# Kernel tuning notes

Measured on AMD Instinct MI355X. Metric: run time of the kernel, lower is better.

Reference implementation:

```python
import jax, jax.numpy as jnp
import numpy as np

B, N, C = 8, 2_000_000, 16


def _per_batch_loss(x, t, num_classes):
    """x: [N] float values, t: [N] int labels.
    For each label group: loss = mean(group) - mode(group) (scipy mode,
    ties -> smallest value), scattered back to every position of that label.
    """
    n = x.shape[0]
    # Sort primarily by label, secondarily by value (lexsort: last key primary).
    order = jnp.lexsort((x, t))
    xs = x[order]
    ts = t[order]
    # Run-length encode equal (label, value) pairs to count value multiplicity.
    new_run = jnp.concatenate(
        [jnp.ones((1,), bool), (ts[1:] != ts[:-1]) | (xs[1:] != xs[:-1])])
    run_id = jnp.cumsum(new_run) - 1                      # [N]
    run_cnt = jax.ops.segment_sum(jnp.ones(n, xs.dtype), run_id,
                                  num_segments=n)[run_id]  # count per element
    # Mode per label = smallest value attaining the max multiplicity.
    grp_max = jax.ops.segment_max(run_cnt, ts, num_segments=num_classes)
    mode = jax.ops.segment_min(
        jnp.where(run_cnt == grp_max[ts], xs, jnp.inf), ts,
        num_segments=num_classes)                         # [C]
    ssum = jax.ops.segment_sum(xs, ts, num_segments=num_classes)
    scnt = jax.ops.segment_sum(jnp.ones(n, xs.dtype), ts,
                               num_segments=num_classes)
    mean = ssum / jnp.maximum(scnt, 1.0)
    per_label = jnp.where(scnt > 0, mean - mode, 0.0)     # [C]
    return per_label[t]                                    # scatter back, [N]


def setup_inputs() -> dict:
    key = jax.random.key(0)
    k1, k2 = jax.random.split(key)
    inputs = jax.random.normal(k1, (B, N), dtype=jnp.float32)
    targets = jax.random.randint(k2, (B, N), 0, C, dtype=jnp.int32)
    return {"inputs": inputs, "targets": targets, "num_classes": C}


def reference(inputs, targets, num_classes):
    per_pos = jax.vmap(lambda x, t: _per_batch_loss(x, t, num_classes))(
        inputs, targets)                                   # [B, N]
    return jnp.mean(per_pos)
```

## Files before the change

### kernel.cpp

```cpp
#include <hip/hip_runtime.h>
#include <stdint.h>

#define NUM_C 16
#define NUM_B 8
#define NBKT (NUM_C * 64)
#define NGRP 256
#define CHUNK_S 4096
#define TAB 4096
#define MAX_NB 8

__device__ __forceinline__ unsigned hash_u32(unsigned h) {
    h ^= h >> 16; h *= 0x85ebca6bu;
    h ^= h >> 13; h *= 0xc2b2ae35u;
    h ^= h >> 16;
    return h;
}
__device__ __forceinline__ unsigned canon_key(float v) {
    unsigned k = __float_as_uint(v);
    return (k == 0x80000000u) ? 0u : k;
}
__device__ __forceinline__ unsigned bucket_of(unsigned key, int c) {
    return ((unsigned)c << 6) | (hash_u32(key) >> 26);
}

__global__ void __launch_bounds__(512)
sort_kernel(const float* __restrict__ x, const int* __restrict__ t,
            long long N, int bbase, int nchunk,
            unsigned* __restrict__ keysout, unsigned short* __restrict__ offs)
{
    __shared__ unsigned hist[NBKT];
    __shared__ unsigned lout[CHUNK_S];
    __shared__ unsigned wsum[8];
    const int lb = blockIdx.x / nchunk;
    const int ch = blockIdx.x % nchunk;
    const int b  = bbase + lb;
    const long long base = (long long)ch * CHUNK_S;
    const int count = (int)((N - base < CHUNK_S) ? (N - base) : CHUNK_S);
    const float* xb = x + (size_t)b * N + base;
    const int*   tb = t + (size_t)b * N + base;
    const int tid = threadIdx.x;

    for (int i = tid; i < NBKT; i += 512) hist[i] = 0u;
    __syncthreads();

    unsigned keys[8], pk[8];
    const int n4 = count >> 2;
    #pragma unroll
    for (int r = 0; r < 2; ++r) {
        const int idx4 = tid + r * 512;
        if (idx4 < n4) {
            float4 v  = ((const float4*)xb)[idx4];
            int4   cc = ((const int4*)tb)[idx4];
            unsigned k0 = canon_key(v.x), b0 = bucket_of(k0, cc.x);
            unsigned k1 = canon_key(v.y), b1 = bucket_of(k1, cc.y);
            unsigned k2 = canon_key(v.z), b2 = bucket_of(k2, cc.z);
            unsigned k3 = canon_key(v.w), b3 = bucket_of(k3, cc.w);
            unsigned p0 = atomicAdd(&hist[b0], 1u);
            unsigned p1 = atomicAdd(&hist[b1], 1u);
            unsigned p2 = atomicAdd(&hist[b2], 1u);
            unsigned p3 = atomicAdd(&hist[b3], 1u);
            keys[r*4+0] = k0; pk[r*4+0] = (b0 << 13) | p0;
            keys[r*4+1] = k1; pk[r*4+1] = (b1 << 13) | p1;
            keys[r*4+2] = k2; pk[r*4+2] = (b2 << 13) | p2;
            keys[r*4+3] = k3; pk[r*4+3] = (b3 << 13) | p3;
        }
    }
    unsigned kex = 0u, pkx = 0u; int hex = 0;
    {
        const int remi = (n4 << 2) + tid;
        if (remi < count) {
            unsigned k = canon_key(xb[remi]);
            unsigned bk = bucket_of(k, tb[remi]);
            unsigned p = atomicAdd(&hist[bk], 1u);
            kex = k; pkx = (bk << 13) | p; hex = 1;
        }
    }
    __syncthreads();

    {
        unsigned b0v = hist[2 * tid], b1v = hist[2 * tid + 1];
        unsigned s = b0v + b1v, inc = s;
        const int lane = tid & 63;
        #pragma unroll
        for (int d = 1; d < 64; d <<= 1) {
            unsigned tt = __shfl_up(inc, d);
            if (lane >= d) inc += tt;
        }
        if (lane == 63) wsum[tid >> 6] = inc;
        __syncthreads();
        unsigned wbase = 0;
        for (int i = 0; i < (tid >> 6); ++i) wbase += wsum[i];
        unsigned excl = wbase + inc - s;
        hist[2 * tid]     = excl + b0v;
        hist[2 * tid + 1] = excl + s;
        __syncthreads();
    }

    #pragma unroll
    for (int r = 0; r < 2; ++r) {
        const int idx4 = tid + r * 512;
        if (idx4 < n4) {
            #pragma unroll
            for (int c2 = 0; c2 < 4; ++c2) {
                unsigned bk = pk[r*4+c2] >> 13, p = pk[r*4+c2] & 8191u;
                lout[(bk ? hist[bk - 1] : 0u) + p] = keys[r*4+c2];
            }
        }
    }
    if (hex) {
        unsigned bk = pkx >> 13, p = pkx & 8191u;
        lout[(bk ? hist[bk - 1] : 0u) + p] = kex;
    }
    __syncthreads();

    unsigned* kb = keysout + (size_t)lb * N + base;
    if (count == CHUNK_S) {
        #pragma unroll
        for (int r = 0; r < 2; ++r)
            ((uint4*)kb)[tid + r * 512] = ((const uint4*)lout)[tid + r * 512];
    } else {
        for (int i = tid; i < count; i += 512) kb[i] = lout[i];
    }
    unsigned short* orow = offs + ((size_t)lb * nchunk + ch) * 1025;
    orow[tid]       = (unsigned short)(tid ? hist[tid - 1] : 0u);
    orow[tid + 512] = (unsigned short)hist[tid + 511];
    if (tid == 0) orow[1024] = (unsigned short)hist[1023];
}

__global__ void __launch_bounds__(256)
transpose_kernel(const unsigned short* __restrict__ offs,
                 unsigned short* __restrict__ offsT, int nchunk, int nchpad)
{
    __shared__ unsigned short tile[32][33];
    const int tiles_r = 33;
    const int tiles_c = (nchunk + 31) >> 5;
    const int lb  = blockIdx.x / (tiles_r * tiles_c);
    const int rem = blockIdx.x % (tiles_r * tiles_c);
    const int r0 = (rem / tiles_c) * 32;
    const int c0 = (rem % tiles_c) * 32;
    const unsigned short* src = offs + (size_t)lb * nchunk * 1025;
    unsigned short* dst = offsT + (size_t)lb * 1025 * nchpad;
    const int tx = threadIdx.x & 31, ty = threadIdx.x >> 5;

    #pragma unroll
    for (int dy = 0; dy < 32; dy += 8) {
        int ch = c0 + ty + dy, row = r0 + tx;
        tile[ty + dy][tx] = (ch < nchunk && row < 1025)
            ? src[(size_t)ch * 1025 + row] : (unsigned short)0;
    }
    __syncthreads();
    #pragma unroll
    for (int dy = 0; dy < 32; dy += 8) {
        int row = r0 + ty + dy, ch = c0 + tx;
        if (row < 1025 && ch < nchpad)
            dst[(size_t)row * nchpad + ch] = tile[tx][ty + dy];
    }
}

__global__ void __launch_bounds__(512)
mode_kernel(const unsigned* __restrict__ keysout,
            const unsigned short* __restrict__ offsT,
            long long N, int nchunk, int nchpad, int bbase,
            unsigned long long* __restrict__ best,
            double* __restrict__ psum,
            unsigned* __restrict__ pcnt)
{
    __shared__ unsigned keyt[TAB];
    __shared__ unsigned cnt16[TAB / 2];
    __shared__ unsigned short rowbuf[5][512];
    __shared__ unsigned long long redb[8];
    __shared__ double reds[8];
    __shared__ unsigned redc[8];

    const unsigned nwg = gridDim.x;
    const unsigned logical = (blockIdx.x & 7u) * (nwg >> 3) + (blockIdx.x >> 3);
    const unsigned lb = logical >> 8;
    const unsigned G  = logical & 255u;
    const unsigned g0 = G << 2;
    const unsigned c  = G >> 4;
    const unsigned b  = (unsigned)bbase + lb;
    const int tid = threadIdx.x;
    const int lane = tid & 63, wid = tid >> 6;

    const uint4 z4 = make_uint4(0u, 0u, 0u, 0u);
    for (int i = tid; i < TAB / 4; i += 512) ((uint4*)keyt)[i] = z4;
    for (int i = tid; i < TAB / 8; i += 512) ((uint4*)cnt16)[i] = z4;

    const unsigned short* obT = offsT + (size_t)lb * 1025 * nchpad;
    for (int i = tid; i < 5 * 512; i += 512) {
        int r = i >> 9, q = i & 511;
        rowbuf[r][q] = (q < nchunk)
            ? obT[(size_t)(g0 + r) * nchpad + q] : (unsigned short)0;
    }
    __syncthreads();

    const unsigned* kb = keysout + (size_t)lb * N;
    double ls = 0.0;
    unsigned mo = 0xFFFFFFFFu;
    unsigned lc = 0u;
    unsigned bc = 0u, bo = 0xFFFFFFFFu;

    const int nit = (nchunk + 127) >> 7;
    for (int sb = 0; sb < 4; ++sb) {
        for (int it = 0; it < nit; ++it) {
            const int q = it * 128 + wid * 16 + (lane >> 2);
            if (q < nchunk) {
                const unsigned s = rowbuf[sb][q];
                const unsigned e = rowbuf[sb + 1][q];
                const unsigned* src = kb + (size_t)q * CHUNK_S;
                for (unsigned jj = s + (unsigned)(lane & 3); jj < e; jj += 4u) {
                    unsigned key = src[jj];
                    ls += (double)__uint_as_float(key);
                    ++lc;
                    unsigned o = (key & 0x80000000u) ? ~key
                                                     : (key | 0x80000000u);
                    if (o < mo) mo = o;
                    unsigned hh = hash_u32(o) & (TAB - 1);
                    unsigned old = atomicCAS(&keyt[hh], 0u, o);
                    unsigned cnt = 1u;
                    while (old != 0u) {
                        if (old == o) {
                            unsigned sh = (hh & 1u) << 4;
                            unsigned ret =
                                atomicAdd(&cnt16[hh >> 1], 1u << sh);
                            cnt = ((ret >> sh) & 0xFFFFu) + 2u;
                            break;
                        }
                        hh = (hh + 1u) & (TAB - 1u);
                        old = atomicCAS(&keyt[hh], 0u, o);
                    }
                    if (cnt >= 2u && (cnt > bc || (cnt == bc && o < bo))) {
                        bc = cnt; bo = o;
                    }
                }
            }
        }
        if (sb < 3) {
            __syncthreads();
            for (int i = tid; i < TAB / 4; i += 512) ((uint4*)keyt)[i] = z4;
            for (int i = tid; i < TAB / 8; i += 512) ((uint4*)cnt16)[i] = z4;
            __syncthreads();
        }
    }

    unsigned long long lbst = bc ? (((unsigned long long)bc << 32)
                                    | (unsigned long long)(~bo)) : 0ull;
    {
        unsigned long long s1 = (1ull << 32) | (unsigned long long)(~mo);
        if (s1 > lbst) lbst = s1;
    }
    #pragma unroll
    for (int sh = 32; sh > 0; sh >>= 1) {
        unsigned long long obv = __shfl_down(lbst, sh);
        if (obv > lbst) lbst = obv;
        ls += __shfl_down(ls, sh);
        lc += __shfl_down(lc, sh);
    }
    if (lane == 0) { redb[wid] = lbst; reds[wid] = ls; redc[wid] = lc; }
    __syncthreads();
    if (tid == 0) {
        unsigned long long bb = 0ull; double ss = 0.0; unsigned cc = 0u;
        #pragma unroll
        for (int i = 0; i < 8; ++i) {
            if (redb[i] > bb) bb = redb[i];
            ss += reds[i];
            cc += redc[i];
        }
        psum[b * NGRP + G] = ss;
        pcnt[b * NGRP + G] = cc;
        if (bb) atomicMax(&best[b * NUM_C + c], bb);
    }
}

__global__ void __launch_bounds__(128)
finalize_kernel(const double* __restrict__ psum,
                const unsigned* __restrict__ pcnt,
                const unsigned long long* __restrict__ best,
                float* __restrict__ out, double inv_total)
{
    __shared__ double acc[NUM_B * NUM_C];
    const int i = threadIdx.x;
    const int b = i >> 4, c = i & 15;

    double s = 0.0;
    unsigned long long cnt = 0ull;
    const double*   ps = psum + (size_t)b * NGRP + ((size_t)c << 4);
    const unsigned* pc = pcnt + (size_t)b * NGRP + ((size_t)c << 4);
    for (int r = 0; r < 16; ++r) { s += ps[r]; cnt += pc[r]; }

    double term = 0.0;
    if (cnt > 0ull) {
        unsigned long long p = best[i];
        unsigned ord = 0xFFFFFFFFu - (unsigned)(p & 0xFFFFFFFFull);
        unsigned ub  = (ord & 0x80000000u) ? (ord ^ 0x80000000u) : ~ord;
        float mode = __uint_as_float(ub);
        term = s - (double)cnt * (double)mode;
    }
    acc[i] = term;
    __syncthreads();
    for (int st = 64; st > 0; st >>= 1) {
        if (i < st) acc[i] += acc[i + st];
        __syncthreads();
    }
    if (i == 0) out[0] = (float)(acc[0] * inv_total);
}

extern "C" void kernel_launch(void* const* d_in, const int* in_sizes, int n_in,
                              void* d_out, int out_size, void* d_ws, size_t ws_size,
                              hipStream_t stream)
{
    const float* x = (const float*)d_in[0];
    const int*   t = (const int*)d_in[1];

    const long long total = in_sizes[0];
    const long long N = total / NUM_B;
    const int nchunk = (int)((N + CHUNK_S - 1) / CHUNK_S);
    const int nchpad = (nchunk + 63) & ~63;

    char* ws = (char*)d_ws;
    size_t off = 0;
    unsigned long long* best = (unsigned long long*)(ws + off);
    off += (size_t)NUM_B * NUM_C * 8;
    double* psum = (double*)(ws + off);
    off += (size_t)NUM_B * NGRP * 8;
    unsigned* pcnt = (unsigned*)(ws + off);
    off += (size_t)NUM_B * NGRP * 4;
    off = (off + 255) & ~(size_t)255;

    const size_t keys_per_b  = (size_t)N * 4;
    const size_t offs_per_b  = (size_t)nchunk * 1025 * 2;
    const size_t offsT_per_b = (size_t)1025 * nchpad * 2;
    const size_t per_b = keys_per_b + offs_per_b + offsT_per_b + 512;
    size_t remaining = ws_size - off;
    int nb = (int)(remaining / per_b);
    if (nb < 1) nb = 1;
    if (nb > MAX_NB) nb = MAX_NB;
    {
        int rounds = (NUM_B + nb - 1) / nb;
        nb = (NUM_B + rounds - 1) / rounds;
    }

    unsigned* keysout = (unsigned*)(ws + off);
    off += (size_t)nb * keys_per_b;
    off = (off + 255) & ~(size_t)255;
    unsigned short* offsA = (unsigned short*)(ws + off);
    off += (size_t)nb * offs_per_b;
    off = (off + 255) & ~(size_t)255;
    unsigned short* offsT = (unsigned short*)(ws + off);
    off += (size_t)nb * offsT_per_b;

    const int tiles = 33 * ((nchunk + 31) >> 5);
    hipMemsetAsync(best, 0, (size_t)NUM_B * NUM_C * 8, stream);
    for (int r = 0; r < NUM_B; r += nb) {
        const int nbr = (NUM_B - r < nb) ? (NUM_B - r) : nb;
        sort_kernel<<<nbr * nchunk, 512, 0, stream>>>(
            x, t, N, r, nchunk, keysout, offsA);
        transpose_kernel<<<nbr * tiles, 256, 0, stream>>>(
            offsA, offsT, nchunk, nchpad);
        mode_kernel<<<nbr * NGRP, 512, 0, stream>>>(
            keysout, offsT, N, nchunk, nchpad, r, best, psum, pcnt);
    }
    finalize_kernel<<<1, 128, 0, stream>>>(
        psum, pcnt, best, (float*)d_out,
        1.0 / ((double)NUM_B * (double)N));
}
```

Before: 276.6 us.

## Use larger hash table with two sub-bucket passes and one thread per chunk

The mode kernel's shared hash table doubles to 8192 slots. Each work-group now handles its four sub-buckets in two passes instead of four, so the table is cleared and synchronised fewer times. Each thread now owns one whole chunk and processes four keys per step, batching loads and the first CAS probes for more memory-level parallelism. The element count comes straight from the offset rows instead of per-element increments. The cost is higher LDS use, which may lower occupancy, and load imbalance when chunk segment lengths differ between threads.

```diff
diff --git a/kernel.cpp b/kernel.cpp
--- a/kernel.cpp
+++ b/kernel.cpp
@@ -6,7 +6,7 @@
 #define NBKT (NUM_C * 64)
 #define NGRP 256
 #define CHUNK_S 4096
-#define TAB 4096
+#define TAB 8192
 #define MAX_NB 8
 
 __device__ __forceinline__ unsigned hash_u32(unsigned h) {
@@ -167,7 +167,7 @@
 {
     __shared__ unsigned keyt[TAB];
     __shared__ unsigned cnt16[TAB / 2];
-    __shared__ unsigned short rowbuf[5][512];
+    __shared__ unsigned short rowbuf[3][512];
     __shared__ unsigned long long redb[8];
     __shared__ double reds[8];
     __shared__ unsigned redc[8];
@@ -187,61 +187,79 @@
     for (int i = tid; i < TAB / 8; i += 512) ((uint4*)cnt16)[i] = z4;
 
     const unsigned short* obT = offsT + (size_t)lb * 1025 * nchpad;
-    for (int i = tid; i < 5 * 512; i += 512) {
-        int r = i >> 9, q = i & 511;
-        rowbuf[r][q] = (q < nchunk)
-            ? obT[(size_t)(g0 + r) * nchpad + q] : (unsigned short)0;
+    for (int i = tid; i < 3 * 512; i += 512) {
+        int r = i >> 9, qq = i & 511;
+        rowbuf[r][qq] = (qq < nchunk)
+            ? obT[(size_t)(g0 + 2 * r) * nchpad + qq] : (unsigned short)0;
     }
     __syncthreads();
 
     const unsigned* kb = keysout + (size_t)lb * N;
     double ls = 0.0;
     unsigned mo = 0xFFFFFFFFu;
-    unsigned lc = 0u;
     unsigned bc = 0u, bo = 0xFFFFFFFFu;
 
-    const int nit = (nchunk + 127) >> 7;
-    for (int sb = 0; sb < 4; ++sb) {
-        for (int it = 0; it < nit; ++it) {
-            const int q = it * 128 + wid * 16 + (lane >> 2);
-            if (q < nchunk) {
-                const unsigned s = rowbuf[sb][q];
-                const unsigned e = rowbuf[sb + 1][q];
-                const unsigned* src = kb + (size_t)q * CHUNK_S;
-                for (unsigned jj = s + (unsigned)(lane & 3); jj < e; jj += 4u) {
-                    unsigned key = src[jj];
+    const unsigned q = (unsigned)tid;
+    const unsigned* src = kb + (size_t)q * CHUNK_S;
+    const bool qok = (q < (unsigned)nchunk);
+
+    for (int ss = 0; ss < 2; ++ss) {
+        unsigned s = 0u, e = 0u;
+        if (qok) { s = rowbuf[ss][q]; e = rowbuf[ss + 1][q]; }
+        if (e > (unsigned)CHUNK_S) e = 0u;
+        if (s > e) s = e;
+        for (unsigned j4 = s; j4 < e; j4 += 4u) {
+            const int nv = (int)((e - j4 < 4u) ? (e - j4) : 4u);
+            unsigned kk[4];
+            #pragma unroll
+            for (int m = 0; m < 4; ++m)
+                kk[m] = (m < nv) ? src[j4 + (unsigned)m] : 0u;
+            unsigned od[4], h[4], old[4];
+            #pragma unroll
+            for (int m = 0; m < 4; ++m) {
+                if (m < nv) {
+                    unsigned key = kk[m];
                     ls += (double)__uint_as_float(key);
-                    ++lc;
                     unsigned o = (key & 0x80000000u) ? ~key
                                                      : (key | 0x80000000u);
                     if (o < mo) mo = o;
-                    unsigned hh = hash_u32(o) & (TAB - 1);
-                    unsigned old = atomicCAS(&keyt[hh], 0u, o);
-                    unsigned cnt = 1u;
-                    while (old != 0u) {
-                        if (old == o) {
-                            unsigned sh = (hh & 1u) << 4;
-                            unsigned ret =
-                                atomicAdd(&cnt16[hh >> 1], 1u << sh);
-                            cnt = ((ret >> sh) & 0xFFFFu) + 2u;
-                            break;
-                        }
-                        hh = (hh + 1u) & (TAB - 1u);
-                        old = atomicCAS(&keyt[hh], 0u, o);
-                    }
-                    if (cnt >= 2u && (cnt > bc || (cnt == bc && o < bo))) {
-                        bc = cnt; bo = o;
-                    }
+                    od[m] = o;
+                    h[m] = hash_u32(o) & (TAB - 1);
                 }
             }
-        }
-        if (sb < 3) {
+            #pragma unroll
+            for (int m = 0; m < 4; ++m)
+                if (m < nv) old[m] = atomicCAS(&keyt[h[m]], 0u, od[m]);
+            #pragma unroll
+            for (int m = 0; m < 4; ++m) {
+                if (m >= nv) continue;
+                unsigned o = old[m], hh = h[m];
+                const unsigned oo = od[m];
+                unsigned cnt = 1u;
+                while (o != 0u) {
+                    if (o == oo) {
+                        unsigned sh = (hh & 1u) << 4;
+                        unsigned ret = atomicAdd(&cnt16[hh >> 1], 1u << sh);
+                        cnt = ((ret >> sh) & 0xFFFFu) + 2u;
+                        break;
+                    }
+                    hh = (hh + 1u) & (TAB - 1u);
+                    o = atomicCAS(&keyt[hh], 0u, oo);
+                }
+                if (cnt >= 2u && (cnt > bc || (cnt == bc && oo < bo))) {
+                    bc = cnt; bo = oo;
+                }
+            }
+        }
+        if (ss == 0) {
             __syncthreads();
             for (int i = tid; i < TAB / 4; i += 512) ((uint4*)keyt)[i] = z4;
             for (int i = tid; i < TAB / 8; i += 512) ((uint4*)cnt16)[i] = z4;
             __syncthreads();
         }
     }
+
+    unsigned lc = qok ? ((unsigned)rowbuf[2][q] - (unsigned)rowbuf[0][q]) : 0u;
 
     unsigned long long lbst = bc ? (((unsigned long long)bc << 32)
                                     | (unsigned long long)(~bo)) : 0ull;
@@ -259,14 +277,14 @@
     if (lane == 0) { redb[wid] = lbst; reds[wid] = ls; redc[wid] = lc; }
     __syncthreads();
     if (tid == 0) {
-        unsigned long long bb = 0ull; double ss = 0.0; unsigned cc = 0u;
+        unsigned long long bb = 0ull; double ss2 = 0.0; unsigned cc = 0u;
         #pragma unroll
         for (int i = 0; i < 8; ++i) {
             if (redb[i] > bb) bb = redb[i];
-            ss += reds[i];
+            ss2 += reds[i];
             cc += redc[i];
         }
-        psum[b * NGRP + G] = ss;
+        psum[b * NGRP + G] = ss2;
         pcnt[b * NGRP + G] = cc;
         if (bb) atomicMax(&best[b * NUM_C + c], bb);
     }
```

Result: slower. 283.2 us (+2.4%).
